# Optimization experiments

Measured on AMD Instinct MI355X. Metric: run time of the kernel, lower is better.

## Reference

```python
import jax, jax.numpy as jnp
import numpy as np

NX, NY, NZ = 432, 496, 1
VX, VY, VZ = 0.16, 0.16, 4.0
XOFF = VX / 2 + 0.0
YOFF = VY / 2 + (-39.68)
ZOFF = VZ / 2 + (-3.0)
GRID = NZ * NX * NY
P, NPT, B = 100000, 32, 8
EPS = 1e-3


def setup_inputs() -> dict:
    key = jax.random.key(0)
    k1, k2, k3, k4 = jax.random.split(key, 4)
    voxels = jax.random.normal(k1, (P, NPT, 4), dtype=jnp.float32)
    num_points = jax.random.randint(k2, (P,), 1, NPT + 1, dtype=jnp.int32)
    b = jax.random.randint(k3, (P,), 0, B, dtype=jnp.int32)
    # unique BEV cells (17 coprime with GRID, P < GRID) -> deterministic scatter
    cell = (jnp.arange(P, dtype=jnp.int32) * 17) % GRID
    y = cell // NX
    x = cell % NX
    coords = jnp.stack([b, jnp.zeros_like(b), y, x], axis=1)  # [P,4] (b,z,y,x)
    W = jax.random.normal(k4, (64, 10), dtype=jnp.float32) * 0.1
    gamma = jnp.ones((64,), dtype=jnp.float32)
    beta = jnp.zeros((64,), dtype=jnp.float32)
    return {"voxels": voxels, "num_points": num_points, "coords": coords,
            "W": W, "gamma": gamma, "beta": beta}


def reference(voxels, num_points, coords, W, gamma, beta):
    cf = coords.astype(voxels.dtype)
    npf = num_points.astype(voxels.dtype)
    # cluster feature: offset from pillar mean
    points_mean = voxels[:, :, :3].sum(axis=1, keepdims=True) / npf[:, None, None]
    f_cluster = voxels[:, :, :3] - points_mean
    # center feature: offset from voxel center
    cx = cf[:, 3, None] * VX + XOFF
    cy = cf[:, 2, None] * VY + YOFF
    cz = cf[:, 1, None] * VZ + ZOFF
    f_center = jnp.stack([voxels[:, :, 0] - cx,
                          voxels[:, :, 1] - cy,
                          voxels[:, :, 2] - cz], axis=-1)
    feat = jnp.concatenate([voxels, f_cluster, f_center], axis=-1)  # [P,N,10]
    mask = (jnp.arange(NPT, dtype=jnp.int32)[None, :] < num_points[:, None])
    feat = feat * mask.astype(feat.dtype)[:, :, None]
    # linear(10->64, no bias) + BatchNorm1d (batch stats, biased var) + relu
    x = jnp.einsum('pnf,cf->pnc', feat, W)  # [P,N,64]
    mean = x.mean(axis=(0, 1))
    var = ((x - mean) ** 2).mean(axis=(0, 1))
    x = (x - mean) * jax.lax.rsqrt(var + EPS) * gamma + beta
    x = jax.nn.relu(x)
    pillars = x.max(axis=1)  # [P,64]
    idx = coords[:, 1] + coords[:, 2] * NX + coords[:, 3]
    bev = jnp.zeros((B, GRID, 64), dtype=pillars.dtype)
    bev = bev.at[coords[:, 0], idx].set(pillars)
    bev = jnp.transpose(bev, (0, 2, 1))  # [B,64,GRID]
    return bev.reshape(B, 64 * NZ, NY, NX)
```

## Files before the change

kernel.cpp:

```cpp
#include <hip/hip_runtime.h>

typedef unsigned short u16;

#define NXg 432
#define NYg 496
#define GRIDg (NXg*NYg)
#define NPTg 32
#define Bg 8
#define CHg 64
#define NSLOT 32

__device__ __forceinline__ float bf2f(u16 u){
    union { unsigned int i; float f; } x; x.i = ((unsigned int)u) << 16; return x.f;
}
__device__ __forceinline__ u16 f2bf(float f){
    union { float f; unsigned int i; } x; x.f = f;
    unsigned int i = x.i + 0x7FFFu + ((x.i >> 16) & 1u);
    return (u16)(i >> 16);
}
__device__ __forceinline__ bool is_bf16(const void* gamma){
    return ((*(const unsigned*)gamma) & 0xFFFFu) != 0u;
}
__device__ __forceinline__ float rdlane(float v, int k){
    return __int_as_float(__builtin_amdgcn_readlane(__float_as_int(v), k));
}

__global__ __launch_bounds__(256) void pfe_init(int* __restrict__ map, float* __restrict__ chsum){
    int t = blockIdx.x*256 + threadIdx.x;
    ((int4*)map)[t] = make_int4(-1,-1,-1,-1);
    if (t < (NSLOT*128)/4) ((float4*)chsum)[t] = make_float4(0.f,0.f,0.f,0.f);
}

__global__ __launch_bounds__(256) void pfe_pillar(
    const void* __restrict__ vox, const int* __restrict__ nump,
    const int* __restrict__ coords, const void* __restrict__ Wv,
    const void* __restrict__ gv,
    u16* __restrict__ pv, int* __restrict__ map, float* __restrict__ chsum,
    int P, int nwaves)
{
    const bool isbf = is_bf16(gv);
    int lane = threadIdx.x & 63;
    int wid  = (blockIdx.x*256 + threadIdx.x) >> 6;
    int n    = lane & 31;

    float w4,w5,w6,w7,w8,w9, wp0,wp1,wp2,wp3;
    bool gsel;
    {
        float w[10];
#pragma unroll
        for (int j=0;j<10;j++)
            w[j] = isbf ? bf2f(((const u16*)Wv)[lane*10 + j]) : ((const float*)Wv)[lane*10 + j];
        wp0 = w[0]+w[4]+w[7];
        wp1 = w[1]+w[5]+w[8];
        wp2 = w[2]+w[6]+w[9];
        wp3 = w[3];
        w4=w[4]; w5=w[5]; w6=w[6]; w7=w[7]; w8=w[8]; w9=w[9];
        float g = isbf ? bf2f(((const u16*)gv)[lane]) : ((const float*)gv)[lane];
        gsel = (g >= 0.f);
    }

    float sx = 0.f, sx2 = 0.f;

    for (int p = wid; p < P; p += nwaves) {
        int np = nump[p];
        int4 cc = *(const int4*)(coords + 4*p);
        float4 pt;
        if (isbf){
            ushort4 raw = *(const ushort4*)((const u16*)vox + ((size_t)p*NPTg + n)*4);
            pt = make_float4(bf2f(raw.x), bf2f(raw.y), bf2f(raw.z), bf2f(raw.w));
        } else {
            pt = *(const float4*)((const float*)vox + ((size_t)p*NPTg + n)*4);
        }

        float s0 = pt.x, s1 = pt.y, s2 = pt.z;
#pragma unroll
        for (int m = 1; m < 32; m <<= 1){
            s0 += __shfl_xor(s0, m, 64);
            s1 += __shfl_xor(s1, m, 64);
            s2 += __shfl_xor(s2, m, 64);
        }
        float inv = 1.0f / (float)np;
        float m0 = s0*inv, m1 = s1*inv, m2 = s2*inv;
        float ccx = (float)cc.w * 0.16f + 0.08f;
        float ccy = (float)cc.z * 0.16f + (0.08f - 39.68f);
        float ccz = (float)cc.y * 4.0f  + (2.0f - 3.0f);
        float d = -(m0*w4 + m1*w5 + m2*w6 + ccx*w7 + ccy*w8 + ccz*w9);

        float qmx = -3e38f, qmn = 3e38f, sq = 0.f, sq2 = 0.f;
        int k = 0;
        for (; k + 4 <= np; k += 4){
#pragma unroll
            for (int u = 0; u < 4; u++){
                float ax = rdlane(pt.x, k+u);
                float ay = rdlane(pt.y, k+u);
                float az = rdlane(pt.z, k+u);
                float aw = rdlane(pt.w, k+u);
                float q = fmaf(ax, wp0, fmaf(ay, wp1, fmaf(az, wp2, aw*wp3)));
                qmx = fmaxf(qmx, q);
                qmn = fminf(qmn, q);
                sq += q;
                sq2 = fmaf(q, q, sq2);
            }
        }
        for (; k < np; k++){
            float ax = rdlane(pt.x, k);
            float ay = rdlane(pt.y, k);
            float az = rdlane(pt.z, k);
            float aw = rdlane(pt.w, k);
            float q = fmaf(ax, wp0, fmaf(ay, wp1, fmaf(az, wp2, aw*wp3)));
            qmx = fmaxf(qmx, q);
            qmn = fminf(qmn, q);
            sq += q;
            sq2 = fmaf(q, q, sq2);
        }

        float npf = (float)np;
        sx  += sq + npf*d;
        sx2 += sq2 + d*(2.f*sq + npf*d);

        float fmx = qmx + d, fmn = qmn + d;
        if (np < NPTg){ fmx = fmaxf(fmx, 0.f); fmn = fminf(fmn, 0.f); }
        pv[(size_t)p*CHg + lane] = f2bf(gsel ? fmx : fmn);
        if (lane == 0) map[cc.x*GRIDg + cc.z*NXg + cc.w] = p;
    }

    float* slot = chsum + (blockIdx.x & (NSLOT-1))*128;
    atomicAdd(slot + lane, sx);
    atomicAdd(slot + 64 + lane, sx2);
}

__global__ __launch_bounds__(64) void pfe_stats(
    const float* __restrict__ chsum,
    const void* __restrict__ gv, const void* __restrict__ bv,
    float* __restrict__ sb, int P)
{
    const bool isbf = is_bf16(gv);
    int t = threadIdx.x;
    float S = 0.f, S2 = 0.f;
    for (int sl = 0; sl < NSLOT; sl++){
        S  += chsum[sl*128 + t];
        S2 += chsum[sl*128 + 64 + t];
    }
    float cnt = (float)P * (float)NPTg;
    float mean = S / cnt;
    float var  = S2 / cnt - mean*mean;
    float g  = isbf ? bf2f(((const u16*)gv)[t]) : ((const float*)gv)[t];
    float be = isbf ? bf2f(((const u16*)bv)[t]) : ((const float*)bv)[t];
    float sc = g * rsqrtf(var + 1e-3f);
    sb[t] = sc; sb[64 + t] = be - mean*sc;
}

__global__ __launch_bounds__(192) void pfe_gather(
    const int* __restrict__ map, const u16* __restrict__ pv,
    const float* __restrict__ sb, const void* __restrict__ gv,
    void* __restrict__ out)
{
    const bool isbf = is_bf16(gv);
    int b  = blockIdx.z;
    int c0 = blockIdx.y * 32;
    int px = blockIdx.x*768 + threadIdx.x*4;
    int4 m4 = *(const int4*)(map + (size_t)b*GRIDg + px);
    int pidx[4] = {m4.x, m4.y, m4.z, m4.w};
    bool val[4];
    uint4 R[4][4];
#pragma unroll
    for (int i = 0; i < 4; i++){
        val[i] = pidx[i] >= 0;
        int p = val[i] ? pidx[i] : 0;
        const uint4* rp = (const uint4*)(pv + (size_t)p*CHg + c0);
        R[i][0] = rp[0]; R[i][1] = rp[1]; R[i][2] = rp[2]; R[i][3] = rp[3];
    }

#pragma unroll
    for (int j = 0; j < 32; j++){
        float sc = sb[c0 + j];
        float bi = sb[64 + c0 + j];
        float r[4];
#pragma unroll
        for (int i = 0; i < 4; i++){
            unsigned dw = ((const unsigned*)R[i])[j >> 1];
            float x = __uint_as_float((j & 1) ? (dw & 0xFFFF0000u) : (dw << 16));
            r[i] = val[i] ? fmaxf(fmaf(sc, x, bi), 0.f) : 0.f;
        }
        size_t obase = ((size_t)(b*CHg + c0 + j))*GRIDg + px;
        if (isbf){
            uint2 pk;
            pk.x = (unsigned)f2bf(r[0]) | ((unsigned)f2bf(r[1]) << 16);
            pk.y = (unsigned)f2bf(r[2]) | ((unsigned)f2bf(r[3]) << 16);
            *(uint2*)((u16*)out + obase) = pk;
        } else {
            float4 o; o.x = r[0]; o.y = r[1]; o.z = r[2]; o.w = r[3];
            *(float4*)((float*)out + obase) = o;
        }
    }
}

extern "C" void kernel_launch(void* const* d_in, const int* in_sizes, int n_in,
                              void* d_out, int out_size, void* d_ws, size_t ws_size,
                              hipStream_t stream)
{
    const void* vox   = d_in[0];
    const int* nump   = (const int*)d_in[1];
    const int* coords = (const int*)d_in[2];
    const void* Wv    = d_in[3];
    const void* gv    = d_in[4];
    const void* bv    = d_in[5];
    int P = in_sizes[1];

    float* chsum = (float*)d_ws;
    float* sb    = (float*)((char*)d_ws + 16384);
    u16*   pv    = (u16*)((char*)d_ws + 32768);
    int*   map   = (int*)((char*)pv + (size_t)P*CHg*2);

    int initThreads = (Bg*GRIDg)/4;
    pfe_init<<<initThreads/256, 256, 0, stream>>>(map, chsum);

    int blocks1 = 2048;
    pfe_pillar<<<blocks1, 256, 0, stream>>>(vox, nump, coords, Wv, gv, pv, map, chsum, P, blocks1*4);

    pfe_stats<<<1, 64, 0, stream>>>(chsum, gv, bv, sb, P);

    dim3 g3(GRIDg/768, 2, Bg);
    pfe_gather<<<g3, 192, 0, stream>>>(map, pv, sb, gv, d_out);
}
```

Before: 539.9 us.

## Apply BN to pillar features before scatter and use LDS for point broadcast

```diff
diff --git a/kernel.cpp b/kernel.cpp
--- a/kernel.cpp
+++ b/kernel.cpp
@@ -21,14 +21,13 @@
 __device__ __forceinline__ bool is_bf16(const void* gamma){
     return ((*(const unsigned*)gamma) & 0xFFFFu) != 0u;
 }
-__device__ __forceinline__ float rdlane(float v, int k){
-    return __int_as_float(__builtin_amdgcn_readlane(__float_as_int(v), k));
-}
-
-__global__ __launch_bounds__(256) void pfe_init(int* __restrict__ map, float* __restrict__ chsum){
+
+__global__ __launch_bounds__(256) void pfe_init(int* __restrict__ map, float* __restrict__ chsum,
+                                                u16* __restrict__ pv, int P){
     int t = blockIdx.x*256 + threadIdx.x;
     ((int4*)map)[t] = make_int4(-1,-1,-1,-1);
     if (t < (NSLOT*128)/4) ((float4*)chsum)[t] = make_float4(0.f,0.f,0.f,0.f);
+    if (t < 8) ((uint4*)(pv + (size_t)P*CHg))[t] = make_uint4(0u,0u,0u,0u);
 }
 
 __global__ __launch_bounds__(256) void pfe_pillar(
@@ -38,9 +37,11 @@
     u16* __restrict__ pv, int* __restrict__ map, float* __restrict__ chsum,
     int P, int nwaves)
 {
+    __shared__ float4 pts[4][32];
     const bool isbf = is_bf16(gv);
     int lane = threadIdx.x & 63;
     int wid  = (blockIdx.x*256 + threadIdx.x) >> 6;
+    int ws   = threadIdx.x >> 6;
     int n    = lane & 31;
 
     float w4,w5,w6,w7,w8,w9, wp0,wp1,wp2,wp3;
@@ -71,6 +72,7 @@
         } else {
             pt = *(const float4*)((const float*)vox + ((size_t)p*NPTg + n)*4);
         }
+        if (lane < 32) pts[ws][n] = pt;
 
         float s0 = pt.x, s1 = pt.y, s2 = pt.z;
 #pragma unroll
@@ -86,16 +88,14 @@
         float ccz = (float)cc.y * 4.0f  + (2.0f - 3.0f);
         float d = -(m0*w4 + m1*w5 + m2*w6 + ccx*w7 + ccy*w8 + ccz*w9);
 
+        const float4* row = pts[ws];
         float qmx = -3e38f, qmn = 3e38f, sq = 0.f, sq2 = 0.f;
         int k = 0;
         for (; k + 4 <= np; k += 4){
 #pragma unroll
             for (int u = 0; u < 4; u++){
-                float ax = rdlane(pt.x, k+u);
-                float ay = rdlane(pt.y, k+u);
-                float az = rdlane(pt.z, k+u);
-                float aw = rdlane(pt.w, k+u);
-                float q = fmaf(ax, wp0, fmaf(ay, wp1, fmaf(az, wp2, aw*wp3)));
+                float4 a = row[k+u];
+                float q = fmaf(a.x, wp0, fmaf(a.y, wp1, fmaf(a.z, wp2, a.w*wp3)));
                 qmx = fmaxf(qmx, q);
                 qmn = fminf(qmn, q);
                 sq += q;
@@ -103,11 +103,8 @@
             }
         }
         for (; k < np; k++){
-            float ax = rdlane(pt.x, k);
-            float ay = rdlane(pt.y, k);
-            float az = rdlane(pt.z, k);
-            float aw = rdlane(pt.w, k);
-            float q = fmaf(ax, wp0, fmaf(ay, wp1, fmaf(az, wp2, aw*wp3)));
+            float4 a = row[k];
+            float q = fmaf(a.x, wp0, fmaf(a.y, wp1, fmaf(a.z, wp2, a.w*wp3)));
             qmx = fmaxf(qmx, q);
             qmn = fminf(qmn, q);
             sq += q;
@@ -150,48 +147,105 @@
     sb[t] = sc; sb[64 + t] = be - mean*sc;
 }
 
+__global__ __launch_bounds__(256) void pfe_postbn(
+    u16* __restrict__ pv, const float* __restrict__ sb,
+    const void* __restrict__ gv, int P)
+{
+    if (!is_bf16(gv)) return;
+    int t = blockIdx.x*256 + threadIdx.x;
+    if (t >= P*8) return;
+    size_t i0 = (size_t)t*8;
+    int c0 = (int)(i0 & 63);
+    uint4 v = *(uint4*)(pv + i0);
+    float4 sA = *(const float4*)(sb + c0);
+    float4 sB = *(const float4*)(sb + c0 + 4);
+    float4 bA = *(const float4*)(sb + 64 + c0);
+    float4 bB = *(const float4*)(sb + 64 + c0 + 4);
+#define PB(dw, slo, blo, shi, bhi) \
+    ( (unsigned)f2bf(fmaxf(fmaf(slo, bf2f((u16)((dw) & 0xFFFFu)), blo), 0.f)) \
+    | ((unsigned)f2bf(fmaxf(fmaf(shi, bf2f((u16)((dw) >> 16)),    bhi), 0.f)) << 16) )
+    unsigned o0 = PB(v.x, sA.x, bA.x, sA.y, bA.y);
+    unsigned o1 = PB(v.y, sA.z, bA.z, sA.w, bA.w);
+    unsigned o2 = PB(v.z, sB.x, bB.x, sB.y, bB.y);
+    unsigned o3 = PB(v.w, sB.z, bB.z, sB.w, bB.w);
+#undef PB
+    *(uint4*)(pv + i0) = make_uint4(o0, o1, o2, o3);
+}
+
 __global__ __launch_bounds__(192) void pfe_gather(
     const int* __restrict__ map, const u16* __restrict__ pv,
     const float* __restrict__ sb, const void* __restrict__ gv,
-    void* __restrict__ out)
+    void* __restrict__ out, int P)
 {
     const bool isbf = is_bf16(gv);
     int b  = blockIdx.z;
     int c0 = blockIdx.y * 32;
     int px = blockIdx.x*768 + threadIdx.x*4;
     int4 m4 = *(const int4*)(map + (size_t)b*GRIDg + px);
-    int pidx[4] = {m4.x, m4.y, m4.z, m4.w};
-    bool val[4];
-    uint4 R[4][4];
-#pragma unroll
-    for (int i = 0; i < 4; i++){
-        val[i] = pidx[i] >= 0;
-        int p = val[i] ? pidx[i] : 0;
-        const uint4* rp = (const uint4*)(pv + (size_t)p*CHg + c0);
-        R[i][0] = rp[0]; R[i][1] = rp[1]; R[i][2] = rp[2]; R[i][3] = rp[3];
-    }
-
-#pragma unroll
-    for (int j = 0; j < 32; j++){
-        float sc = sb[c0 + j];
-        float bi = sb[64 + c0 + j];
-        float r[4];
-#pragma unroll
-        for (int i = 0; i < 4; i++){
-            unsigned dw = ((const unsigned*)R[i])[j >> 1];
-            float x = __uint_as_float((j & 1) ? (dw & 0xFFFF0000u) : (dw << 16));
-            r[i] = val[i] ? fmaxf(fmaf(sc, x, bi), 0.f) : 0.f;
-        }
-        size_t obase = ((size_t)(b*CHg + c0 + j))*GRIDg + px;
-        if (isbf){
-            uint2 pk;
-            pk.x = (unsigned)f2bf(r[0]) | ((unsigned)f2bf(r[1]) << 16);
-            pk.y = (unsigned)f2bf(r[2]) | ((unsigned)f2bf(r[3]) << 16);
-            *(uint2*)((u16*)out + obase) = pk;
-        } else {
-            float4 o; o.x = r[0]; o.y = r[1]; o.z = r[2]; o.w = r[3];
-            *(float4*)((float*)out + obase) = o;
-        }
+
+    if (isbf){
+        int p0 = (m4.x < 0) ? P : m4.x;
+        int p1 = (m4.y < 0) ? P : m4.y;
+        int p2 = (m4.z < 0) ? P : m4.z;
+        int p3 = (m4.w < 0) ? P : m4.w;
+        const uint4* r0 = (const uint4*)(pv + (size_t)p0*CHg + c0);
+        const uint4* r1 = (const uint4*)(pv + (size_t)p1*CHg + c0);
+        const uint4* r2 = (const uint4*)(pv + (size_t)p2*CHg + c0);
+        const uint4* r3 = (const uint4*)(pv + (size_t)p3*CHg + c0);
+        uint4 A0=r0[0], A1=r0[1], A2=r0[2], A3=r0[3];
+        uint4 B0=r1[0], B1=r1[1], B2=r1[2], B3=r1[3];
+        uint4 C0=r2[0], C1=r2[1], C2=r2[2], C3=r2[3];
+        uint4 D0=r3[0], D1=r3[1], D2=r3[2], D3=r3[3];
+        u16* ob = (u16*)out + ((size_t)(b*CHg + c0))*GRIDg + px;
+#define GETB(Q0,Q1,Q2,Q3, COMP, CREL) { \
+        unsigned w0=Q0.COMP, w1=Q1.COMP, w2=Q2.COMP, w3=Q3.COMP; \
+        uint2 e, o; \
+        e.x = __builtin_amdgcn_perm(w1, w0, 0x05040100u); \
+        e.y = __builtin_amdgcn_perm(w3, w2, 0x05040100u); \
+        o.x = __builtin_amdgcn_perm(w1, w0, 0x07060302u); \
+        o.y = __builtin_amdgcn_perm(w3, w2, 0x07060302u); \
+        *(uint2*)(ob + (size_t)(CREL)*GRIDg)     = e; \
+        *(uint2*)(ob + (size_t)((CREL)+1)*GRIDg) = o; }
+        GETB(A0,B0,C0,D0, x, 0)  GETB(A0,B0,C0,D0, y, 2)  GETB(A0,B0,C0,D0, z, 4)  GETB(A0,B0,C0,D0, w, 6)
+        GETB(A1,B1,C1,D1, x, 8)  GETB(A1,B1,C1,D1, y, 10) GETB(A1,B1,C1,D1, z, 12) GETB(A1,B1,C1,D1, w, 14)
+        GETB(A2,B2,C2,D2, x, 16) GETB(A2,B2,C2,D2, y, 18) GETB(A2,B2,C2,D2, z, 20) GETB(A2,B2,C2,D2, w, 22)
+        GETB(A3,B3,C3,D3, x, 24) GETB(A3,B3,C3,D3, y, 26) GETB(A3,B3,C3,D3, z, 28) GETB(A3,B3,C3,D3, w, 30)
+#undef GETB
+    } else {
+        bool v0 = m4.x >= 0, v1 = m4.y >= 0, v2 = m4.z >= 0, v3 = m4.w >= 0;
+        int p0 = v0 ? m4.x : 0;
+        int p1 = v1 ? m4.y : 0;
+        int p2 = v2 ? m4.z : 0;
+        int p3 = v3 ? m4.w : 0;
+        const uint4* r0 = (const uint4*)(pv + (size_t)p0*CHg + c0);
+        const uint4* r1 = (const uint4*)(pv + (size_t)p1*CHg + c0);
+        const uint4* r2 = (const uint4*)(pv + (size_t)p2*CHg + c0);
+        const uint4* r3 = (const uint4*)(pv + (size_t)p3*CHg + c0);
+        uint4 A0=r0[0], A1=r0[1], A2=r0[2], A3=r0[3];
+        uint4 B0=r1[0], B1=r1[1], B2=r1[2], B3=r1[3];
+        uint4 C0=r2[0], C1=r2[1], C2=r2[2], C3=r2[3];
+        uint4 D0=r3[0], D1=r3[1], D2=r3[2], D3=r3[3];
+        float* obf = (float*)out + ((size_t)(b*CHg + c0))*GRIDg + px;
+#define GETF(Q0,Q1,Q2,Q3, COMP, CREL) { \
+        unsigned w0=Q0.COMP, w1=Q1.COMP, w2=Q2.COMP, w3=Q3.COMP; \
+        float sce = sb[c0+(CREL)],   bie = sb[64+c0+(CREL)]; \
+        float sco = sb[c0+(CREL)+1], bio = sb[64+c0+(CREL)+1]; \
+        float4 oe, oo; \
+        oe.x = v0 ? fmaxf(fmaf(sce, __uint_as_float(w0 << 16), bie), 0.f) : 0.f; \
+        oe.y = v1 ? fmaxf(fmaf(sce, __uint_as_float(w1 << 16), bie), 0.f) : 0.f; \
+        oe.z = v2 ? fmaxf(fmaf(sce, __uint_as_float(w2 << 16), bie), 0.f) : 0.f; \
+        oe.w = v3 ? fmaxf(fmaf(sce, __uint_as_float(w3 << 16), bie), 0.f) : 0.f; \
+        oo.x = v0 ? fmaxf(fmaf(sco, __uint_as_float(w0 & 0xFFFF0000u), bio), 0.f) : 0.f; \
+        oo.y = v1 ? fmaxf(fmaf(sco, __uint_as_float(w1 & 0xFFFF0000u), bio), 0.f) : 0.f; \
+        oo.z = v2 ? fmaxf(fmaf(sco, __uint_as_float(w2 & 0xFFFF0000u), bio), 0.f) : 0.f; \
+        oo.w = v3 ? fmaxf(fmaf(sco, __uint_as_float(w3 & 0xFFFF0000u), bio), 0.f) : 0.f; \
+        *(float4*)(obf + (size_t)(CREL)*GRIDg)     = oe; \
+        *(float4*)(obf + (size_t)((CREL)+1)*GRIDg) = oo; }
+        GETF(A0,B0,C0,D0, x, 0)  GETF(A0,B0,C0,D0, y, 2)  GETF(A0,B0,C0,D0, z, 4)  GETF(A0,B0,C0,D0, w, 6)
+        GETF(A1,B1,C1,D1, x, 8)  GETF(A1,B1,C1,D1, y, 10) GETF(A1,B1,C1,D1, z, 12) GETF(A1,B1,C1,D1, w, 14)
+        GETF(A2,B2,C2,D2, x, 16) GETF(A2,B2,C2,D2, y, 18) GETF(A2,B2,C2,D2, z, 20) GETF(A2,B2,C2,D2, w, 22)
+        GETF(A3,B3,C3,D3, x, 24) GETF(A3,B3,C3,D3, y, 26) GETF(A3,B3,C3,D3, z, 28) GETF(A3,B3,C3,D3, w, 30)
+#undef GETF
     }
 }
 
@@ -210,16 +264,19 @@
     float* chsum = (float*)d_ws;
     float* sb    = (float*)((char*)d_ws + 16384);
     u16*   pv    = (u16*)((char*)d_ws + 32768);
-    int*   map   = (int*)((char*)pv + (size_t)P*CHg*2);
+    int*   map   = (int*)((char*)pv + (size_t)(P+1)*CHg*2);
 
     int initThreads = (Bg*GRIDg)/4;
-    pfe_init<<<initThreads/256, 256, 0, stream>>>(map, chsum);
+    pfe_init<<<initThreads/256, 256, 0, stream>>>(map, chsum, pv, P);
 
     int blocks1 = 2048;
     pfe_pillar<<<blocks1, 256, 0, stream>>>(vox, nump, coords, Wv, gv, pv, map, chsum, P, blocks1*4);
 
     pfe_stats<<<1, 64, 0, stream>>>(chsum, gv, bv, sb, P);
 
+    int pbBlocks = (P*8 + 255)/256;
+    pfe_postbn<<<pbBlocks, 256, 0, stream>>>(pv, sb, gv, P);
+
     dim3 g3(GRIDg/768, 2, Bg);
-    pfe_gather<<<g3, 192, 0, stream>>>(map, pv, sb, gv, d_out);
-}
+    pfe_gather<<<g3, 192, 0, stream>>>(map, pv, sb, gv, d_out, P);
+}
```

Measured after the change: 520.5 us. 3.6% less time.
